# Optimization experiments

Hardware: AMD Instinct MI355X
Metric: run time of the kernel (lower is better)

Reference implementation:

```python
import jax, jax.numpy as jnp
import numpy as np

N = 100000
E = 1600000
C = 128  # in_channels == hidden_channels
L = 4    # num_layers
EPS = 1e-5


def _bn_eval(x, g, b, m, v):
    # BatchNorm in eval mode: use running statistics
    return (x - m) * (g / jnp.sqrt(v + EPS)) + b


def _sage(x, src, dst, Wl, Wr, b):
    # PyG SAGEConv with mean aggregation: out = lin_l(mean_{j->i} x_j) + lin_r(x_i)
    msg = x[src]                                                  # [E, C] gather
    agg = jax.ops.segment_sum(msg, dst, num_segments=N)           # [N, C] scatter-add
    cnt = jax.ops.segment_sum(jnp.ones((src.shape[0], 1), x.dtype), dst, num_segments=N)
    mean = agg / jnp.maximum(cnt, 1.0)
    return mean @ Wl + x @ Wr + b


def setup_inputs() -> dict:
    key = jax.random.key(0)
    ks = jax.random.split(key, 12)
    s = 1.0 / np.sqrt(C)
    inp = {
        "x": jax.random.normal(ks[0], (N, C), jnp.float32),
        "edge_index": jax.random.randint(ks[1], (2, E), 0, N, jnp.int64),
        # stacked per-layer SAGEConv params (all layers are [C, C] since in==hidden)
        "Wl": jax.random.uniform(ks[2], (L, C, C), jnp.float32, -s, s),
        "Wr": jax.random.uniform(ks[3], (L, C, C), jnp.float32, -s, s),
        "bconv": jnp.zeros((L, C), jnp.float32),
        # per-layer BatchNorm (eval): gamma, beta, running mean/var
        "bn_g": jnp.ones((L, C), jnp.float32),
        "bn_b": jnp.zeros((L, C), jnp.float32),
        "bn_m": jax.random.normal(ks[4], (L, C), jnp.float32) * 0.1,
        "bn_v": jax.random.uniform(ks[5], (L, C), jnp.float32, 0.5, 1.5),
        # final LayerNorm
        "ln_g": jnp.ones((C,), jnp.float32),
        "ln_b": jnp.zeros((C,), jnp.float32),
        # head: lin1 (C -> C//2), bn_out, lin2 (C//2 -> 1)
        "W1": jax.random.uniform(ks[6], (C, C // 2), jnp.float32, -s, s),
        "b1": jnp.zeros((C // 2,), jnp.float32),
        "bo_g": jnp.ones((C // 2,), jnp.float32),
        "bo_b": jnp.zeros((C // 2,), jnp.float32),
        "bo_m": jax.random.normal(ks[7], (C // 2,), jnp.float32) * 0.1,
        "bo_v": jax.random.uniform(ks[8], (C // 2,), jnp.float32, 0.5, 1.5),
        "W2": jax.random.uniform(ks[9], (C // 2, 1), jnp.float32, -1.0 / np.sqrt(C // 2), 1.0 / np.sqrt(C // 2)),
        "b2": jnp.zeros((1,), jnp.float32),
    }
    return inp


def reference(x, edge_index, Wl, Wr, bconv, bn_g, bn_b, bn_m, bn_v,
              ln_g, ln_b, W1, b1, bo_g, bo_b, bo_m, bo_v, W2, b2):
    src, dst = edge_index[0], edge_index[1]
    residual = x
    h = x
    for i in range(L):  # small fixed layer count
        h = _sage(h, src, dst, Wl[i], Wr[i], bconv[i])
        h = _bn_eval(h, bn_g[i], bn_b[i], bn_m[i], bn_v[i])
        h = jax.nn.relu(h)
        # dropout is identity in eval mode
        if i == 0:
            h = h + residual  # shapes match since in_channels == hidden_channels
    # LayerNorm over feature dim
    mu = jnp.mean(h, axis=-1, keepdims=True)
    var = jnp.mean((h - mu) ** 2, axis=-1, keepdims=True)
    h = (h - mu) / jnp.sqrt(var + EPS) * ln_g + ln_b
    # MLP head
    h = _bn_eval(h @ W1 + b1, bo_g, bo_b, bo_m, bo_v)
    h = jax.nn.relu(h)
    out = (h @ W2 + b2)[:, 0]  # squeeze(-1) -> [N]
    return out
```

## Files before the change

kernel.cpp:

```cpp
#include <hip/hip_runtime.h>

#define NN 100000
#define EE 1600000
#define CC 128
#define EPS 1e-5f
#define DMAX 64

typedef __attribute__((ext_vector_type(8))) short sh8;
typedef __attribute__((ext_vector_type(4))) float fl4;

static __device__ __forceinline__ unsigned short f2bf(float f) {
    unsigned u = __float_as_uint(f);
    u = (u + 0x7fff + ((u >> 16) & 1)) >> 16;
    return (unsigned short)u;
}
static __device__ __forceinline__ float bf2f(unsigned short s) {
    return __uint_as_float((unsigned)s << 16);
}

__global__ __launch_bounds__(256) void k_filld(const int* __restrict__ ei,
                                               int* __restrict__ cnt,
                                               int* __restrict__ colp) {
    int e = blockIdx.x * 256 + threadIdx.x;
    if (e < EE) {
        int d = ei[EE + e];
        int pos = atomicAdd(&cnt[d], 1);
        if (pos < DMAX) colp[(size_t)d * DMAX + pos] = ei[e];
    }
}

__global__ __launch_bounds__(256) void k_cvtx(const float* __restrict__ x,
                                              unsigned short* __restrict__ A2) {
    int id = blockIdx.x * 256 + threadIdx.x;
    if (id >= NN * CC / 8) return;
    int row = id >> 4, g = id & 15;
    const float* xp = x + (size_t)row * CC + g * 8;
    unsigned short o[8];
#pragma unroll
    for (int e = 0; e < 8; ++e) o[e] = f2bf(xp[e]);
    *(sh8*)(A2 + (size_t)row * 256 + 128 + g * 8) = *(sh8*)o;
}

__global__ __launch_bounds__(256) void k_wcvt(const float* __restrict__ Wl,
                                              const float* __restrict__ Wr,
                                              unsigned short* __restrict__ Wfrag) {
    int id = blockIdx.x * 256 + threadIdx.x;
    if (id >= 16384) return;
    int lay = id >> 12;
    int rem = id & 4095;
    int ks = rem >> 9;
    int nt = (rem >> 6) & 7;
    int l = rem & 63;
    int c = nt * 16 + (l & 15);
    int kb = ks * 32 + (l >> 4) * 8;
    const float* WL = Wl + (size_t)lay * CC * CC;
    const float* WR = Wr + (size_t)lay * CC * CC;
    unsigned short o[8];
#pragma unroll
    for (int e = 0; e < 8; ++e) {
        int k = kb + e;
        float v = (k < 128) ? WL[(size_t)k * CC + c] : WR[(size_t)(k - 128) * CC + c];
        o[e] = f2bf(v);
    }
    *(sh8*)(Wfrag + (size_t)lay * 32768 + ks * 4096 + nt * 512 + l * 8) = *(sh8*)o;
}

__global__ __launch_bounds__(256) void k_gather(const int* __restrict__ cnt,
                                                const int* __restrict__ colp,
                                                unsigned short* __restrict__ A2) {
    int node = blockIdx.x * 4 + (threadIdx.x >> 6);
    if (node >= NN) return;
    int lane = threadIdx.x & 63;
    int g = lane & 15;
    int par = lane >> 4;
    const unsigned short* hbase = A2 + 128 + g * 8;
    const int* cl = colp + (size_t)node * DMAX;
    int c = cnt[node];
    if (c > DMAX) c = DMAX;
    float acc[8];
#pragma unroll
    for (int e = 0; e < 8; ++e) acc[e] = 0.f;
    int j = par;
    for (; j + 4 < c; j += 8) {
        int s0 = cl[j];
        int s1 = cl[j + 4];
        sh8 v0 = *(const sh8*)(hbase + (size_t)s0 * 256);
        sh8 v1 = *(const sh8*)(hbase + (size_t)s1 * 256);
#pragma unroll
        for (int e = 0; e < 8; ++e) acc[e] += bf2f((unsigned short)v0[e]);
#pragma unroll
        for (int e = 0; e < 8; ++e) acc[e] += bf2f((unsigned short)v1[e]);
    }
    if (j < c) {
        int s0 = cl[j];
        sh8 v0 = *(const sh8*)(hbase + (size_t)s0 * 256);
#pragma unroll
        for (int e = 0; e < 8; ++e) acc[e] += bf2f((unsigned short)v0[e]);
    }
#pragma unroll
    for (int e = 0; e < 8; ++e) {
        acc[e] += __shfl_xor(acc[e], 16);
        acc[e] += __shfl_xor(acc[e], 32);
    }
    if (par == 0) {
        float sc = 1.0f / fmaxf((float)c, 1.0f);
        unsigned short o[8];
#pragma unroll
        for (int e = 0; e < 8; ++e) o[e] = f2bf(acc[e] * sc);
        *(sh8*)(A2 + (size_t)node * 256 + g * 8) = *(sh8*)o;
    }
}

__global__ __launch_bounds__(256) void k_gemm(
    const unsigned short* __restrict__ A2w,
    unsigned short* __restrict__ A2,
    const unsigned short* __restrict__ Wfrag,
    const float* __restrict__ bconv,
    const float* __restrict__ bng, const float* __restrict__ bnb,
    const float* __restrict__ bnm, const float* __restrict__ bnv,
    const float* __restrict__ x, int add_res)
{
    const int t = threadIdx.x;
    const int w = t >> 6, l = t & 63;
    const int rowbase = blockIdx.x * 64 + w * 16;
    int r_a = rowbase + (l & 15);
    if (r_a >= NN) r_a = NN - 1;
    const unsigned short* arow = A2w + (size_t)r_a * 256 + (l >> 4) * 8;

    fl4 acc[8];
#pragma unroll
    for (int nt = 0; nt < 8; ++nt) acc[nt] = (fl4){0.f, 0.f, 0.f, 0.f};

#pragma unroll
    for (int ks = 0; ks < 8; ++ks) {
        sh8 a = *(const sh8*)(arow + ks * 32);
        const unsigned short* wk = Wfrag + ks * 4096 + l * 8;
#pragma unroll
        for (int nt = 0; nt < 8; ++nt) {
            sh8 b = *(const sh8*)(wk + nt * 512);
            acc[nt] = __builtin_amdgcn_mfma_f32_16x16x32_bf16(a, b, acc[nt], 0, 0, 0);
        }
    }

    const int r0 = rowbase + (l >> 4) * 4;
#pragma unroll
    for (int nt = 0; nt < 8; ++nt) {
        int c = nt * 16 + (l & 15);
        float sc = bng[c] * rsqrtf(bnv[c] + EPS);
        float tt = (bconv[c] - bnm[c]) * sc + bnb[c];
#pragma unroll
        for (int j = 0; j < 4; ++j) {
            int row = r0 + j;
            if (row < NN) {
                float v = acc[nt][j] * sc + tt;
                v = fmaxf(v, 0.f);
                if (add_res) v += x[(size_t)row * CC + c];
                A2[(size_t)row * 256 + 128 + c] = f2bf(v);
            }
        }
    }
}

__global__ __launch_bounds__(256) void k_head2(
    const unsigned short* __restrict__ A2,
    const float* __restrict__ lng, const float* __restrict__ lnb,
    const float* __restrict__ W1, const float* __restrict__ b1,
    const float* __restrict__ bog, const float* __restrict__ bob,
    const float* __restrict__ bom, const float* __restrict__ bov,
    const float* __restrict__ W2, const float* __restrict__ b2,
    float* __restrict__ out)
{
    __shared__ float Ws[128][68];
    __shared__ float hs[32][132];
    const int t = threadIdx.x;
    const int nbase = blockIdx.x * 32;

#pragma unroll
    for (int i = 0; i < 8; ++i) {
        int fi = (t + i * 256) * 4;
        int k = fi >> 6, j = fi & 63;
        *(float4*)&Ws[k][j] = *(const float4*)(W1 + fi);
    }

    const int lane = t & 63, wv = t >> 6;
#pragma unroll
    for (int i = 0; i < 8; ++i) {
        int nl = wv * 8 + i;
        const unsigned short* hp = A2 + (size_t)(nbase + nl) * 256 + 128;
        float v0 = bf2f(hp[lane]), v1 = bf2f(hp[lane + 64]);
        float s1 = v0 + v1, s2 = v0 * v0 + v1 * v1;
#pragma unroll
        for (int o = 32; o >= 1; o >>= 1) {
            s1 += __shfl_xor(s1, o);
            s2 += __shfl_xor(s2, o);
        }
        float mean = s1 * (1.0f / 128.0f);
        float var = s2 * (1.0f / 128.0f) - mean * mean;
        float rstd = rsqrtf(var + EPS);
        hs[nl][lane] = (v0 - mean) * rstd * lng[lane] + lnb[lane];
        hs[nl][lane + 64] = (v1 - mean) * rstd * lng[lane + 64] + lnb[lane + 64];
    }
    __syncthreads();

    const int tx = t & 15, ty = t >> 4;
    const int c0 = tx * 4, r0 = ty * 2;
    float acc[2][4] = {{0.f, 0.f, 0.f, 0.f}, {0.f, 0.f, 0.f, 0.f}};
#pragma unroll 4
    for (int k = 0; k < 128; k += 4) {
        float4 w0 = *(const float4*)&Ws[k][c0];
        float4 w1 = *(const float4*)&Ws[k + 1][c0];
        float4 w2v = *(const float4*)&Ws[k + 2][c0];
        float4 w3 = *(const float4*)&Ws[k + 3][c0];
#pragma unroll
        for (int i = 0; i < 2; ++i) {
            float4 a = *(const float4*)&hs[r0 + i][k];
            acc[i][0] += a.x * w0.x + a.y * w1.x + a.z * w2v.x + a.w * w3.x;
            acc[i][1] += a.x * w0.y + a.y * w1.y + a.z * w2v.y + a.w * w3.y;
            acc[i][2] += a.x * w0.z + a.y * w1.z + a.z * w2v.z + a.w * w3.z;
            acc[i][3] += a.x * w0.w + a.y * w1.w + a.z * w2v.w + a.w * w3.w;
        }
    }

    float rr[2] = {0.f, 0.f};
#pragma unroll
    for (int jc = 0; jc < 4; ++jc) {
        int c = c0 + jc;
        float sc = bog[c] * rsqrtf(bov[c] + EPS);
        float tt = (b1[c] - bom[c]) * sc + bob[c];
        float w2 = W2[c];
#pragma unroll
        for (int i = 0; i < 2; ++i) {
            float v = acc[i][jc] * sc + tt;
            v = fmaxf(v, 0.f);
            rr[i] += v * w2;
        }
    }
#pragma unroll
    for (int i = 0; i < 2; ++i) {
        rr[i] += __shfl_xor(rr[i], 1);
        rr[i] += __shfl_xor(rr[i], 2);
        rr[i] += __shfl_xor(rr[i], 4);
        rr[i] += __shfl_xor(rr[i], 8);
    }
    if (tx == 0) {
        float bb = b2[0];
        out[nbase + r0] = rr[0] + bb;
        out[nbase + r0 + 1] = rr[1] + bb;
    }
}

extern "C" void kernel_launch(void* const* d_in, const int* in_sizes, int n_in,
                              void* d_out, int out_size, void* d_ws, size_t ws_size,
                              hipStream_t stream) {
    const float* x     = (const float*)d_in[0];
    const int*   ei    = (const int*)d_in[1];
    const float* Wl    = (const float*)d_in[2];
    const float* Wr    = (const float*)d_in[3];
    const float* bconv = (const float*)d_in[4];
    const float* bng   = (const float*)d_in[5];
    const float* bnb   = (const float*)d_in[6];
    const float* bnm   = (const float*)d_in[7];
    const float* bnv   = (const float*)d_in[8];
    const float* lng   = (const float*)d_in[9];
    const float* lnb   = (const float*)d_in[10];
    const float* W1    = (const float*)d_in[11];
    const float* b1    = (const float*)d_in[12];
    const float* bog   = (const float*)d_in[13];
    const float* bob   = (const float*)d_in[14];
    const float* bom   = (const float*)d_in[15];
    const float* bov   = (const float*)d_in[16];
    const float* W2    = (const float*)d_in[17];
    const float* b2    = (const float*)d_in[18];

    unsigned short* A2    = (unsigned short*)d_ws;
    unsigned short* Wfrag = A2 + (size_t)NN * 256;
    int*   cnt  = (int*)(Wfrag + 4 * 32768);
    int*   colp = cnt + NN;

    hipMemsetAsync(cnt, 0, NN * sizeof(int), stream);
    k_cvtx<<<(NN * CC / 8 + 255) / 256, 256, 0, stream>>>(x, A2);
    k_wcvt<<<64, 256, 0, stream>>>(Wl, Wr, Wfrag);
    k_filld<<<(EE + 255) / 256, 256, 0, stream>>>(ei, cnt, colp);

    for (int l = 0; l < 4; ++l) {
        k_gather<<<(NN + 3) / 4, 256, 0, stream>>>(cnt, colp, A2);
        k_gemm<<<(NN + 63) / 64, 256, 0, stream>>>(
            A2, A2, Wfrag + (size_t)l * 32768,
            bconv + l * CC, bng + l * CC, bnb + l * CC, bnm + l * CC, bnv + l * CC,
            x, (l == 0) ? 1 : 0);
    }
    k_head2<<<NN / 32, 256, 0, stream>>>(A2, lng, lnb, W1, b1,
                                         bog, bob, bom, bov, W2, b2, (float*)d_out);
}
```

Baseline: 554.3 us.

## Fuse neighbor mean-gather into SAGE GEMM kernel with ping-pong feature buffers

Merges the per-layer gather kernel into the GEMM kernel. Each 64-node block first computes the mean of its neighbor features into LDS, then feeds the MFMA from LDS for the aggregated half and from global memory for the self half. Features move from one interleaved [N,256] buffer to two [N,128] ping-pong buffers. This avoids writing and re-reading the aggregated features through global memory and removes one launch per layer. In exchange, each block now does its gathers serially per wave (16 nodes each), which may cost latency hiding and occupancy compared with the standalone gather grid.

```diff
diff --git a/kernel.cpp b/kernel.cpp
--- a/kernel.cpp
+++ b/kernel.cpp
@@ -30,7 +30,7 @@
 }
 
 __global__ __launch_bounds__(256) void k_cvtx(const float* __restrict__ x,
-                                              unsigned short* __restrict__ A2) {
+                                              unsigned short* __restrict__ h) {
     int id = blockIdx.x * 256 + threadIdx.x;
     if (id >= NN * CC / 8) return;
     int row = id >> 4, g = id & 15;
@@ -38,7 +38,7 @@
     unsigned short o[8];
 #pragma unroll
     for (int e = 0; e < 8; ++e) o[e] = f2bf(xp[e]);
-    *(sh8*)(A2 + (size_t)row * 256 + 128 + g * 8) = *(sh8*)o;
+    *(sh8*)(h + (size_t)row * CC + g * 8) = *(sh8*)o;
 }
 
 __global__ __launch_bounds__(256) void k_wcvt(const float* __restrict__ Wl,
@@ -65,67 +65,73 @@
     *(sh8*)(Wfrag + (size_t)lay * 32768 + ks * 4096 + nt * 512 + l * 8) = *(sh8*)o;
 }
 
-__global__ __launch_bounds__(256) void k_gather(const int* __restrict__ cnt,
-                                                const int* __restrict__ colp,
-                                                unsigned short* __restrict__ A2) {
-    int node = blockIdx.x * 4 + (threadIdx.x >> 6);
-    if (node >= NN) return;
-    int lane = threadIdx.x & 63;
-    int g = lane & 15;
-    int par = lane >> 4;
-    const unsigned short* hbase = A2 + 128 + g * 8;
-    const int* cl = colp + (size_t)node * DMAX;
-    int c = cnt[node];
-    if (c > DMAX) c = DMAX;
-    float acc[8];
-#pragma unroll
-    for (int e = 0; e < 8; ++e) acc[e] = 0.f;
-    int j = par;
-    for (; j + 4 < c; j += 8) {
-        int s0 = cl[j];
-        int s1 = cl[j + 4];
-        sh8 v0 = *(const sh8*)(hbase + (size_t)s0 * 256);
-        sh8 v1 = *(const sh8*)(hbase + (size_t)s1 * 256);
-#pragma unroll
-        for (int e = 0; e < 8; ++e) acc[e] += bf2f((unsigned short)v0[e]);
-#pragma unroll
-        for (int e = 0; e < 8; ++e) acc[e] += bf2f((unsigned short)v1[e]);
-    }
-    if (j < c) {
-        int s0 = cl[j];
-        sh8 v0 = *(const sh8*)(hbase + (size_t)s0 * 256);
-#pragma unroll
-        for (int e = 0; e < 8; ++e) acc[e] += bf2f((unsigned short)v0[e]);
-    }
-#pragma unroll
-    for (int e = 0; e < 8; ++e) {
-        acc[e] += __shfl_xor(acc[e], 16);
-        acc[e] += __shfl_xor(acc[e], 32);
-    }
-    if (par == 0) {
-        float sc = 1.0f / fmaxf((float)c, 1.0f);
-        unsigned short o[8];
-#pragma unroll
-        for (int e = 0; e < 8; ++e) o[e] = f2bf(acc[e] * sc);
-        *(sh8*)(A2 + (size_t)node * 256 + g * 8) = *(sh8*)o;
-    }
-}
-
-__global__ __launch_bounds__(256) void k_gemm(
-    const unsigned short* __restrict__ A2w,
-    unsigned short* __restrict__ A2,
+__global__ __launch_bounds__(256) void k_gg(
+    const int* __restrict__ cnt, const int* __restrict__ colp,
+    const unsigned short* __restrict__ hin,
+    unsigned short* __restrict__ hout,
     const unsigned short* __restrict__ Wfrag,
     const float* __restrict__ bconv,
     const float* __restrict__ bng, const float* __restrict__ bnb,
     const float* __restrict__ bnm, const float* __restrict__ bnv,
     const float* __restrict__ x, int add_res)
 {
+    __shared__ unsigned short mlds[64][132];
     const int t = threadIdx.x;
     const int w = t >> 6, l = t & 63;
-    const int rowbase = blockIdx.x * 64 + w * 16;
+    const int nbase = blockIdx.x * 64;
+
+    {
+        const int g = l & 15;
+        const int par = l >> 4;
+        const unsigned short* hbase = hin + g * 8;
+#pragma unroll 1
+        for (int i = 0; i < 16; ++i) {
+            int node = nbase + w * 16 + i;
+            float acc[8];
+#pragma unroll
+            for (int e = 0; e < 8; ++e) acc[e] = 0.f;
+            if (node < NN) {
+                const int* cl = colp + (size_t)node * DMAX;
+                int c = cnt[node];
+                if (c > DMAX) c = DMAX;
+                int j = par;
+                for (; j + 4 < c; j += 8) {
+                    int s0 = cl[j];
+                    int s1 = cl[j + 4];
+                    sh8 v0 = *(const sh8*)(hbase + (size_t)s0 * CC);
+                    sh8 v1 = *(const sh8*)(hbase + (size_t)s1 * CC);
+#pragma unroll
+                    for (int e = 0; e < 8; ++e) acc[e] += bf2f((unsigned short)v0[e]);
+#pragma unroll
+                    for (int e = 0; e < 8; ++e) acc[e] += bf2f((unsigned short)v1[e]);
+                }
+                if (j < c) {
+                    int s0 = cl[j];
+                    sh8 v0 = *(const sh8*)(hbase + (size_t)s0 * CC);
+#pragma unroll
+                    for (int e = 0; e < 8; ++e) acc[e] += bf2f((unsigned short)v0[e]);
+                }
+#pragma unroll
+                for (int e = 0; e < 8; ++e) {
+                    acc[e] += __shfl_xor(acc[e], 16);
+                    acc[e] += __shfl_xor(acc[e], 32);
+                }
+                if (par == 0) {
+                    float sc = 1.0f / fmaxf((float)c, 1.0f);
+                    unsigned short o[8];
+#pragma unroll
+                    for (int e = 0; e < 8; ++e) o[e] = f2bf(acc[e] * sc);
+                    *(sh8*)&mlds[w * 16 + i][g * 8] = *(sh8*)o;
+                }
+            }
+        }
+    }
+    __syncthreads();
+
+    const int rowbase = nbase + w * 16;
     int r_a = rowbase + (l & 15);
     if (r_a >= NN) r_a = NN - 1;
-    const unsigned short* arow = A2w + (size_t)r_a * 256 + (l >> 4) * 8;
+    const unsigned short* hrow = hin + (size_t)r_a * CC + (l >> 4) * 8;
 
     fl4 acc[8];
 #pragma unroll
@@ -133,7 +139,11 @@
 
 #pragma unroll
     for (int ks = 0; ks < 8; ++ks) {
-        sh8 a = *(const sh8*)(arow + ks * 32);
+        sh8 a;
+        if (ks < 4)
+            a = *(const sh8*)&mlds[w * 16 + (l & 15)][ks * 32 + (l >> 4) * 8];
+        else
+            a = *(const sh8*)(hrow + (ks - 4) * 32);
         const unsigned short* wk = Wfrag + ks * 4096 + l * 8;
 #pragma unroll
         for (int nt = 0; nt < 8; ++nt) {
@@ -155,14 +165,14 @@
                 float v = acc[nt][j] * sc + tt;
                 v = fmaxf(v, 0.f);
                 if (add_res) v += x[(size_t)row * CC + c];
-                A2[(size_t)row * 256 + 128 + c] = f2bf(v);
+                hout[(size_t)row * CC + c] = f2bf(v);
             }
         }
     }
 }
 
 __global__ __launch_bounds__(256) void k_head2(
-    const unsigned short* __restrict__ A2,
+    const unsigned short* __restrict__ h,
     const float* __restrict__ lng, const float* __restrict__ lnb,
     const float* __restrict__ W1, const float* __restrict__ b1,
     const float* __restrict__ bog, const float* __restrict__ bob,
@@ -186,7 +196,7 @@
 #pragma unroll
     for (int i = 0; i < 8; ++i) {
         int nl = wv * 8 + i;
-        const unsigned short* hp = A2 + (size_t)(nbase + nl) * 256 + 128;
+        const unsigned short* hp = h + (size_t)(nbase + nl) * CC;
         float v0 = bf2f(hp[lane]), v1 = bf2f(hp[lane + 64]);
         float s1 = v0 + v1, s2 = v0 * v0 + v1 * v1;
 #pragma unroll
@@ -272,23 +282,26 @@
     const float* W2    = (const float*)d_in[17];
     const float* b2    = (const float*)d_in[18];
 
-    unsigned short* A2    = (unsigned short*)d_ws;
-    unsigned short* Wfrag = A2 + (size_t)NN * 256;
+    unsigned short* hA    = (unsigned short*)d_ws;
+    unsigned short* hB    = hA + (size_t)NN * CC;
+    unsigned short* Wfrag = hB + (size_t)NN * CC;
     int*   cnt  = (int*)(Wfrag + 4 * 32768);
     int*   colp = cnt + NN;
 
     hipMemsetAsync(cnt, 0, NN * sizeof(int), stream);
-    k_cvtx<<<(NN * CC / 8 + 255) / 256, 256, 0, stream>>>(x, A2);
+    k_cvtx<<<(NN * CC / 8 + 255) / 256, 256, 0, stream>>>(x, hA);
     k_wcvt<<<64, 256, 0, stream>>>(Wl, Wr, Wfrag);
     k_filld<<<(EE + 255) / 256, 256, 0, stream>>>(ei, cnt, colp);
 
+    const unsigned short* hin = hA;
+    unsigned short* houts[4] = {hB, hA, hB, hA};
     for (int l = 0; l < 4; ++l) {
-        k_gather<<<(NN + 3) / 4, 256, 0, stream>>>(cnt, colp, A2);
-        k_gemm<<<(NN + 63) / 64, 256, 0, stream>>>(
-            A2, A2, Wfrag + (size_t)l * 32768,
+        k_gg<<<(NN + 63) / 64, 256, 0, stream>>>(
+            cnt, colp, hin, houts[l], Wfrag + (size_t)l * 32768,
             bconv + l * CC, bng + l * CC, bnb + l * CC, bnm + l * CC, bnv + l * CC,
             x, (l == 0) ? 1 : 0);
-    }
-    k_head2<<<NN / 32, 256, 0, stream>>>(A2, lng, lnb, W1, b1,
+        hin = houts[l];
+    }
+    k_head2<<<NN / 32, 256, 0, stream>>>(hA, lng, lnb, W1, b1,
                                          bog, bob, bom, bov, W2, b2, (float*)d_out);
 }
```

Result: slower. 630.5 us (+13.7%).
